# Kernel tuning notes

Measured on AMD Instinct MI355X. Metric: run time of the kernel, lower is better.

Reference implementation:

```python
import jax, jax.numpy as jnp
import numpy as np

PRIME = 2147483647  # 2^31 - 1, MinHash modulus
GAMMA = 0.3
NUM_HEADS = 8


def minhash_sketch(ids, a, b):
    # ids: (B, L, S) int64 atom ids; a,b: (K,) hash coefficients
    # h[b,l,s,k] = (a[k]*id + b[k]) mod PRIME ; signature = min over the set axis S
    h = (ids[..., None] * a + b) % PRIME          # (B, L, S, K)
    return h.min(axis=2)                          # (B, L, K)


def jaccard_from_signatures(sig_q, sig_k):
    # sig_q: (B, Lq, K), sig_k: (B, Lk, K) -> (B, Lq, Lk) fraction of matching slots.
    # Scan over the K hash slots to avoid materializing a (B,Lq,Lk,K) tensor.
    B, Lq, K = sig_q.shape
    Lk = sig_k.shape[1]

    def step(acc, cols):
        qc, kc = cols                              # (B,Lq), (B,Lk)
        return acc + (qc[:, :, None] == kc[:, None, :]).astype(jnp.float32), None

    init = jnp.zeros((B, Lq, Lk), jnp.float32)
    xs = (jnp.moveaxis(sig_q, -1, 0), jnp.moveaxis(sig_k, -1, 0))
    acc, _ = jax.lax.scan(step, init, xs)
    return acc / K


def symdiff_from_jaccard(jacc, size_q, size_k):
    # |A ∩ B| = J/(1+J) * (|A|+|B|)  =>  |A Δ B| = (|A|+|B|) * (1-J)/(1+J)
    tot = size_q[:, :, None] + size_k[:, None, :]   # (B, Lq, Lk)
    return tot * (1.0 - jacc) / (1.0 + jacc)


def setup_inputs() -> dict:
    key = jax.random.key(0)
    ks = jax.random.split(key, 12)
    B, Lq, Lk, E, S, K, V = 4, 1024, 1024, 512, 8, 128, 32000
    w = lambda k: (jax.random.normal(k, (E, E), jnp.float32) * 0.02)
    return {
        "query": jax.random.normal(ks[0], (B, Lq, E), jnp.float32),
        "key": jax.random.normal(ks[1], (B, Lk, E), jnp.float32),
        "value": jax.random.normal(ks[2], (B, Lk, E), jnp.float32),
        "token_sets_q": jax.random.randint(ks[3], (B, Lq, S), 0, V).astype(jnp.int64),
        "token_sets_k": jax.random.randint(ks[4], (B, Lk, S), 0, V).astype(jnp.int64),
        "hash_a": jax.random.randint(ks[5], (K,), 1, PRIME - 1).astype(jnp.int64),
        "hash_b": jax.random.randint(ks[6], (K,), 0, PRIME - 1).astype(jnp.int64),
        "Wq": w(ks[7]), "bq": jnp.zeros((E,), jnp.float32),
        "Wk": w(ks[8]), "bk": jnp.zeros((E,), jnp.float32),
        "Wv": w(ks[9]), "bv": jnp.zeros((E,), jnp.float32),
        "Wo": w(ks[10]), "bo": jnp.zeros((E,), jnp.float32),
    }


def reference(query, key, value, token_sets_q, token_sets_k, hash_a, hash_b,
              Wq, bq, Wk, bk, Wv, bv, Wo, bo):
    B, Lq, E = query.shape
    Lk = key.shape[1]
    H = NUM_HEADS
    d = E // H

    # in-projections (torch Linear: x @ W^T + b); q,k are computed but the
    # attention scores come solely from the token-set kernel (gating disabled)
    q = query @ Wq.T + bq
    k = key @ Wk.T + bk
    v = (value @ Wv.T + bv).reshape(B, Lk, H, d).transpose(0, 2, 1, 3)  # (B,H,Lk,d)

    # MinHash sketches of per-token atom sets -> estimated Jaccard -> Δ-RBF score
    sig_q = minhash_sketch(token_sets_q, hash_a, hash_b)   # (B,Lq,K)
    sig_k = minhash_sketch(token_sets_k, hash_a, hash_b)   # (B,Lk,K)
    jacc = jaccard_from_signatures(sig_q, sig_k)           # (B,Lq,Lk)

    S = token_sets_q.shape[-1]
    size_q = jnp.full((B, Lq), S, jnp.float32)             # uniform CSR offsets -> |set| = S
    size_k = jnp.full((B, Lk), S, jnp.float32)
    delta = symdiff_from_jaccard(jacc, size_q, size_k)
    scores = jnp.exp(-GAMMA * delta)                       # (B,Lq,Lk), shared by all heads

    attn = jax.nn.softmax(scores, axis=-1)                 # no masks, no causal, dropout=0
    ctx = jnp.einsum('bqk,bhkd->bqhd', attn, v).reshape(B, Lq, E)
    return ctx @ Wo.T + bo
```

## Files before the change

### kernel.cpp

```cpp
#include <hip/hip_runtime.h>
#include <hip/hip_bf16.h>
#include <stdint.h>

#define PRIME 2147483647u
#define GAMMA 0.3f
#define K_HASH 128
#define S_SET 8
#define NB 4
#define LQ 1024
#define LK 1024
#define EDIM 512

typedef unsigned short ushort_t;
typedef __attribute__((ext_vector_type(8))) short short8;
typedef __attribute__((ext_vector_type(4))) float f32x4;

static __device__ __forceinline__ unsigned short f2bf(float f) {
    unsigned u = __builtin_bit_cast(unsigned, f);
    u += 0x7FFFu + ((u >> 16) & 1u);
    return (unsigned short)(u >> 16);
}

static __device__ __forceinline__ void glds16(const void* g, void* l) {
    __builtin_amdgcn_global_load_lds(
        (const __attribute__((address_space(1))) unsigned int*)g,
        (__attribute__((address_space(3))) unsigned int*)l, 16, 0, 0);
}

#define SWZ(r) ((((r) >> 2) & 3) ^ ((r) & 3))

#define EPI_ROWBIAS  0
#define EPI_ROWDIV   1
#define EPI_COLBIAS  2

template<int OUTF32, int MODE>
static __device__ void gemm64_dev(
        const ushort_t* __restrict__ A, const ushort_t* __restrict__ B,
        void* __restrict__ C,
        const float* __restrict__ bias, const float* __restrict__ scale,
        int lda, int ldb, int ldc, int Kd, int m0, int n0,
        ushort_t* AsBase, ushort_t* BsBase, int tid) {
    ushort_t (*As)[64 * 32] = (ushort_t (*)[64 * 32])AsBase;
    ushort_t (*Bs)[64 * 32] = (ushort_t (*)[64 * 32])BsBase;
    int w = tid >> 6, lane = tid & 63;
    int wm = (w & 1) * 32, wn = (w >> 1) * 32;
    int mrow = lane & 15, kg = lane >> 4;

    int r = tid >> 2, c = (tid & 3) ^ SWZ(r);
    const ushort_t* pa = A + (size_t)(m0 + r) * lda + c * 8;
    const ushort_t* pb = B + (size_t)(n0 + r) * ldb + c * 8;

    int aoff[2], boff[2];
    #pragma unroll
    for (int s = 0; s < 2; s++) {
        int Ra = wm + s * 16 + mrow;
        aoff[s] = Ra * 32 + (kg ^ SWZ(Ra)) * 8;
        int Rb = wn + s * 16 + mrow;
        boff[s] = Rb * 32 + (kg ^ SWZ(Rb)) * 8;
    }

    f32x4 acc[2][2] = {};
    int nK = Kd >> 5;
    glds16(pa, &As[0][tid * 8]);
    glds16(pb, &Bs[0][tid * 8]);
    for (int i = 0; i < nK; i++) {
        __syncthreads();
        int cur = i & 1, nxt = cur ^ 1;
        if (i + 1 < nK) {
            int k0 = (i + 1) << 5;
            glds16(pa + k0, &As[nxt][tid * 8]);
            glds16(pb + k0, &Bs[nxt][tid * 8]);
        }
        short8 af[2], bh[2];
        #pragma unroll
        for (int s = 0; s < 2; s++) {
            af[s] = *(const short8*)&As[cur][aoff[s]];
            bh[s] = *(const short8*)&Bs[cur][boff[s]];
        }
        #pragma unroll
        for (int ii = 0; ii < 2; ii++)
            #pragma unroll
            for (int jj = 0; jj < 2; jj++)
                acc[ii][jj] = __builtin_amdgcn_mfma_f32_16x16x32_bf16(
                                  af[ii], bh[jj], acc[ii][jj], 0, 0, 0);
    }

    int col = lane & 15, rbase = (lane >> 4) * 4;
    #pragma unroll
    for (int ii = 0; ii < 2; ii++) {
        #pragma unroll
        for (int jj = 0; jj < 2; jj++) {
            #pragma unroll
            for (int rr = 0; rr < 4; rr++) {
                int gm = m0 + wm + ii * 16 + rbase + rr;
                int gn = n0 + wn + jj * 16 + col;
                float v = acc[ii][jj][rr];
                if (MODE == EPI_ROWBIAS)     v += bias[gm];
                else if (MODE == EPI_ROWDIV) v /= scale[gm];
                else                         v += bias[gn];
                size_t cix = (size_t)gm * ldc + gn;
                if (OUTF32) ((float*)C)[cix] = v;
                else        ((ushort_t*)C)[cix] = f2bf(v);
            }
        }
    }
}

#define CVT_N0 (NB * LK * EDIM)
#define CVT_N1 (EDIM * EDIM)
#define CVT_N2 (EDIM * EDIM)
#define CVT_BLOCKS ((CVT_N0 + CVT_N1 + CVT_N2) / (256 * 8))
#define MZ_BLOCKS 1024
#define SIG_BLOCKS (NB * (LQ + LK) / 2)

__global__ __launch_bounds__(256) void prep_kernel(
        const float* __restrict__ v, const float* __restrict__ wv,
        const float* __restrict__ wo,
        ushort_t* __restrict__ vb, ushort_t* __restrict__ wvb,
        ushort_t* __restrict__ wob,
        const int* __restrict__ ts_q, const int* __restrict__ ts_k,
        const int* __restrict__ ha, const int* __restrict__ hb,
        unsigned* __restrict__ sig_q, unsigned* __restrict__ sig_k,
        uint8_t* __restrict__ Mz) {
    int blk = blockIdx.x;
    if (blk < CVT_BLOCKS) {
        size_t i = ((size_t)blk * 256 + threadIdx.x) * 8;
        const float* src; ushort_t* dst; size_t off;
        if (i < CVT_N0)                { src = v;  dst = vb;  off = i; }
        else if (i < CVT_N0 + CVT_N1)  { src = wv; dst = wvb; off = i - CVT_N0; }
        else                           { src = wo; dst = wob; off = i - CVT_N0 - CVT_N1; }
        float4 a = *(const float4*)(src + off);
        float4 b = *(const float4*)(src + off + 4);
        ushort4 o0, o1;
        o0.x = f2bf(a.x); o0.y = f2bf(a.y); o0.z = f2bf(a.z); o0.w = f2bf(a.w);
        o1.x = f2bf(b.x); o1.y = f2bf(b.y); o1.z = f2bf(b.z); o1.w = f2bf(b.w);
        *(ushort4*)(dst + off)     = o0;
        *(ushort4*)(dst + off + 4) = o1;
        return;
    }
    if (blk < CVT_BLOCKS + MZ_BLOCKS) {
        size_t off = ((size_t)(blk - CVT_BLOCKS) * 256 + threadIdx.x) * 16;
        *(int4*)(Mz + off) = (int4){0, 0, 0, 0};
        return;
    }
    int sb = blk - CVT_BLOCKS - MZ_BLOCKS;
    int half = threadIdx.x >> 7, k = threadIdx.x & 127;
    int row = sb * 2 + half;
    const int* ts = (row < NB * LQ) ? ts_q : ts_k;
    unsigned* sig = (row < NB * LQ) ? sig_q : sig_k;
    int idx = row & (NB * LQ - 1);
    unsigned long long a  = (unsigned)ha[k];
    unsigned long long bb = (unsigned)hb[k];
    __shared__ int ids[2][S_SET];
    if (k < S_SET) ids[half][k] = ts[idx * S_SET + k];
    __syncthreads();
    unsigned mn = 0xFFFFFFFFu;
    #pragma unroll
    for (int s = 0; s < S_SET; s++) {
        unsigned long long x = a * (unsigned long long)(unsigned)ids[half][s] + bb;
        x = (x & PRIME) + (x >> 31);
        x = (x & PRIME) + (x >> 31);
        unsigned r = (unsigned)x;
        if (r >= PRIME) r -= PRIME;
        mn = (r < mn) ? r : mn;
    }
    sig[idx * K_HASH + k] = mn;
}

union JSmem {
    struct { unsigned keys[2048]; ushort_t vals[2048]; } j;
    struct { ushort_t As[2][64 * 32]; ushort_t Bs[2][64 * 32]; } g;
};

__global__ __launch_bounds__(256) void joing1_kernel(
        const unsigned* __restrict__ sig_q, const unsigned* __restrict__ sig_k,
        uint8_t* __restrict__ M,
        const ushort_t* __restrict__ Wvb, const ushort_t* __restrict__ Vb,
        ushort_t* __restrict__ Vt, const float* __restrict__ bv) {
    __shared__ JSmem sm;
    int blk = blockIdx.x, tid = threadIdx.x;
    int t = blk & 511;
    if ((blk >> 9) == 0) {
        gemm64_dev<0, EPI_ROWBIAS>(Wvb, Vb, Vt, bv, nullptr,
                                   EDIM, EDIM, NB * LK, EDIM,
                                   (t >> 6) * 64, (t & 63) * 64,
                                   sm.g.As[0], sm.g.Bs[0], tid);
        return;
    }
    int b = t >> 7, k = t & 127;
    for (int i = tid; i < 2048; i += 256) sm.j.keys[i] = 0xFFFFFFFFu;
    __syncthreads();
    const unsigned* skc = sig_k + (size_t)b * LK * K_HASH + k;
    const unsigned* sqc = sig_q + (size_t)b * LQ * K_HASH + k;
    for (int u = 0; u < 4; u++) {
        int j = u * 256 + tid;
        unsigned vv = skc[(size_t)j * K_HASH];
        unsigned h = (vv * 2654435761u) >> 21;
        while (true) {
            unsigned prev = atomicCAS(&sm.j.keys[h], 0xFFFFFFFFu, vv);
            if (prev == 0xFFFFFFFFu) { sm.j.vals[h] = (ushort_t)j; break; }
            h = (h + 1) & 2047;
        }
    }
    __syncthreads();
    uint8_t* Mb = M + ((size_t)b << 20);
    for (int u = 0; u < 4; u++) {
        int q = u * 256 + tid;
        unsigned vv = sqc[(size_t)q * K_HASH];
        unsigned h = (vv * 2654435761u) >> 21;
        unsigned kk;
        while ((kk = sm.j.keys[h]) != 0xFFFFFFFFu) {
            if (kk == vv) {
                unsigned ix = ((unsigned)q << 10) + sm.j.vals[h];
                atomicAdd((unsigned*)(Mb + (ix & ~3u)), 1u << ((ix & 3u) * 8));
            }
            h = (h + 1) & 2047;
        }
    }
}

__global__ __launch_bounds__(256) void lutrs_kernel(
        const uint8_t* __restrict__ M, ushort_t* __restrict__ P,
        float* __restrict__ rs) {
    __shared__ float lut[K_HASH + 1];
    __shared__ float wsum[4];
    int row = blockIdx.x, tid = threadIdx.x;
    if (tid <= K_HASH) {
        float r = (float)(K_HASH - tid) / (float)(K_HASH + tid);
        lut[tid] = expf(expf(-GAMMA * (2.0f * S_SET) * r));
    }
    __syncthreads();
    uchar4 m4 = *(const uchar4*)(M + (size_t)row * LK + tid * 4);
    float p0 = lut[m4.x], p1 = lut[m4.y], p2 = lut[m4.z], p3 = lut[m4.w];
    ushort4 o;
    o.x = f2bf(p0); o.y = f2bf(p1); o.z = f2bf(p2); o.w = f2bf(p3);
    *(ushort4*)(P + (size_t)row * LK + tid * 4) = o;
    float s = (p0 + p1) + (p2 + p3);
    #pragma unroll
    for (int off = 32; off; off >>= 1) s += __shfl_down(s, off);
    if ((tid & 63) == 0) wsum[tid >> 6] = s;
    __syncthreads();
    if (tid == 0) rs[row] = (wsum[0] + wsum[1]) + (wsum[2] + wsum[3]);
}

template<int OUTF32, int MODE>
__global__ __launch_bounds__(256) void btgemm_kernel(
        const ushort_t* __restrict__ A, const ushort_t* __restrict__ B,
        void* __restrict__ C,
        const float* __restrict__ bias, const float* __restrict__ scale,
        int lda, int ldb, int ldc, int Kd,
        long long sA, long long sB, long long sC, long long sS) {
    __shared__ ushort_t As[2][64 * 32], Bs[2][64 * 32];
    int z = blockIdx.z;
    gemm64_dev<OUTF32, MODE>(
        A + (size_t)z * sA, B + (size_t)z * sB,
        (char*)C + (size_t)z * sC * (OUTF32 ? 4 : 2),
        bias, scale + (size_t)z * sS,
        lda, ldb, ldc, Kd, blockIdx.y * 64, blockIdx.x * 64,
        As[0], Bs[0], threadIdx.x);
}

extern "C" void kernel_launch(void* const* d_in, const int* in_sizes, int n_in,
                              void* d_out, int out_size, void* d_ws, size_t ws_size,
                              hipStream_t stream) {
    const float* value = (const float*)d_in[2];
    const int* tsq = (const int*)d_in[3];
    const int* tsk = (const int*)d_in[4];
    const int* ha  = (const int*)d_in[5];
    const int* hb  = (const int*)d_in[6];
    const float* Wv = (const float*)d_in[11];
    const float* bv = (const float*)d_in[12];
    const float* Wo = (const float*)d_in[13];
    const float* bo = (const float*)d_in[14];
    float* out = (float*)d_out;

    char* ws = (char*)d_ws;
    unsigned* sigq = (unsigned*)(ws);
    unsigned* sigk = (unsigned*)(ws + (2ull << 20));
    uint8_t*  M    = (uint8_t*)(ws + (4ull << 20));
    ushort_t* P    = (ushort_t*)(ws + (8ull << 20));
    float*    rs   = (float*)(ws + (16ull << 20));
    ushort_t* Vt   = (ushort_t*)(ws + (16ull << 20) + (64ull << 10));
    ushort_t* ctx  = (ushort_t*)(ws);
    ushort_t* Vb   = (ushort_t*)(ws + (20ull << 20) + (64ull << 10));
    ushort_t* Wvb  = (ushort_t*)(ws + (24ull << 20) + (64ull << 10));
    ushort_t* Wob  = (ushort_t*)(ws + (24ull << 20) + (64ull << 10) + (512ull << 10));

    prep_kernel<<<CVT_BLOCKS + MZ_BLOCKS + SIG_BLOCKS, 256, 0, stream>>>(
        value, Wv, Wo, Vb, Wvb, Wob, tsq, tsk, ha, hb, sigq, sigk, M);

    joing1_kernel<<<1024, 256, 0, stream>>>(sigq, sigk, M, Wvb, Vb, Vt, bv);

    lutrs_kernel<<<NB * LQ, 256, 0, stream>>>(M, P, rs);

    btgemm_kernel<0, EPI_ROWDIV><<<dim3(EDIM / 64, LQ / 64, NB), 256, 0, stream>>>(
        P, Vt, ctx, bv , rs,
        LK, NB * LK, EDIM, LK,
        (long long)LQ * LK, (long long)LK, (long long)LQ * EDIM, (long long)LQ);

    btgemm_kernel<1, EPI_COLBIAS><<<dim3(EDIM / 64, NB * LQ / 64, 1), 256, 0, stream>>>(
        ctx, Wob, out, bo, rs ,
        EDIM, EDIM, EDIM, EDIM, 0LL, 0LL, 0LL, 0LL);
}
```

Baseline: 151.4 us.

## Fold Wo into V projection and replace dense LUT pass with sparse fixups

Reassociates the output projection so that Wo·(Wv·V) is precomputed as W2t, which removes the separate ctx GEMM; the score GEMM then writes the final fp32 output with a divide-by-rowsum plus bias epilogue. P and rowsums are prefilled with the zero-match score. The join records the first hit of each nonzero match cell in a fixlist, and a sparse fixup pass patches P and rowsums, replacing the dense LUT/rowsum kernel. The join also loads four hash slots per block with vector loads. This adds atomics on a global counter and a large fixlist buffer, and it changes the rounding order (bf16 of W2t and Vproj).

```diff
diff --git a/kernel.cpp b/kernel.cpp
--- a/kernel.cpp
+++ b/kernel.cpp
@@ -10,6 +10,7 @@
 #define LQ 1024
 #define LK 1024
 #define EDIM 512
+#define FIX_CAP (NB * LQ * LK)
 
 typedef unsigned short ushort_t;
 typedef __attribute__((ext_vector_type(8))) short short8;
@@ -29,9 +30,15 @@
 
 #define SWZ(r) ((((r) >> 2) & 3) ^ ((r) & 3))
 
+static __device__ __forceinline__ float score_of(int m) {
+    float r = (float)(K_HASH - m) / (float)(K_HASH + m);
+    return expf(expf(-GAMMA * (2.0f * S_SET) * r));
+}
+
 #define EPI_ROWBIAS  0
-#define EPI_ROWDIV   1
 #define EPI_COLBIAS  2
+#define EPI_NONE     3
+#define EPI_DIVBIAS  4
 
 template<int OUTF32, int MODE>
 static __device__ void gemm64_dev(
@@ -95,9 +102,9 @@
                 int gm = m0 + wm + ii * 16 + rbase + rr;
                 int gn = n0 + wn + jj * 16 + col;
                 float v = acc[ii][jj][rr];
-                if (MODE == EPI_ROWBIAS)     v += bias[gm];
-                else if (MODE == EPI_ROWDIV) v /= scale[gm];
-                else                         v += bias[gn];
+                if (MODE == EPI_ROWBIAS)      v += bias[gm];
+                else if (MODE == EPI_COLBIAS) v += bias[gn];
+                else if (MODE == EPI_DIVBIAS) v = v / scale[gm] + bias[gn];
                 size_t cix = (size_t)gm * ldc + gn;
                 if (OUTF32) ((float*)C)[cix] = v;
                 else        ((ushort_t*)C)[cix] = f2bf(v);
@@ -110,8 +117,11 @@
 #define CVT_N1 (EDIM * EDIM)
 #define CVT_N2 (EDIM * EDIM)
 #define CVT_BLOCKS ((CVT_N0 + CVT_N1 + CVT_N2) / (256 * 8))
+#define PF_BLOCKS 2048
 #define MZ_BLOCKS 1024
+#define RS_BLOCKS 16
 #define SIG_BLOCKS (NB * (LQ + LK) / 2)
+#define PREP_GRID (CVT_BLOCKS + PF_BLOCKS + MZ_BLOCKS + RS_BLOCKS + SIG_BLOCKS)
 
 __global__ __launch_bounds__(256) void prep_kernel(
         const float* __restrict__ v, const float* __restrict__ wv,
@@ -121,7 +131,8 @@
         const int* __restrict__ ts_q, const int* __restrict__ ts_k,
         const int* __restrict__ ha, const int* __restrict__ hb,
         unsigned* __restrict__ sig_q, unsigned* __restrict__ sig_k,
-        uint8_t* __restrict__ Mz) {
+        uint8_t* __restrict__ M, ushort_t* __restrict__ P,
+        float* __restrict__ rs, unsigned* __restrict__ nfix) {
     int blk = blockIdx.x;
     if (blk < CVT_BLOCKS) {
         size_t i = ((size_t)blk * 256 + threadIdx.x) * 8;
@@ -138,12 +149,25 @@
         *(ushort4*)(dst + off + 4) = o1;
         return;
     }
-    if (blk < CVT_BLOCKS + MZ_BLOCKS) {
+    if (blk < CVT_BLOCKS + PF_BLOCKS) {
+        unsigned short pb = f2bf(score_of(0));
+        unsigned wpat = (unsigned)pb | ((unsigned)pb << 16);
         size_t off = ((size_t)(blk - CVT_BLOCKS) * 256 + threadIdx.x) * 16;
-        *(int4*)(Mz + off) = (int4){0, 0, 0, 0};
-        return;
-    }
-    int sb = blk - CVT_BLOCKS - MZ_BLOCKS;
+        *(int4*)((char*)P + off) = (int4){(int)wpat, (int)wpat, (int)wpat, (int)wpat};
+        return;
+    }
+    if (blk < CVT_BLOCKS + PF_BLOCKS + MZ_BLOCKS) {
+        size_t off = ((size_t)(blk - CVT_BLOCKS - PF_BLOCKS) * 256 + threadIdx.x) * 16;
+        *(int4*)(M + off) = (int4){0, 0, 0, 0};
+        return;
+    }
+    if (blk < CVT_BLOCKS + PF_BLOCKS + MZ_BLOCKS + RS_BLOCKS) {
+        int i = (blk - CVT_BLOCKS - PF_BLOCKS - MZ_BLOCKS) * 256 + threadIdx.x;
+        rs[i] = (float)LK * score_of(0);
+        if (i == 0) *nfix = 0u;
+        return;
+    }
+    int sb = blk - (CVT_BLOCKS + PF_BLOCKS + MZ_BLOCKS + RS_BLOCKS);
     int half = threadIdx.x >> 7, k = threadIdx.x & 127;
     int row = sb * 2 + half;
     const int* ts = (row < NB * LQ) ? ts_q : ts_k;
@@ -172,75 +196,105 @@
     struct { ushort_t As[2][64 * 32]; ushort_t Bs[2][64 * 32]; } g;
 };
 
+static __device__ __forceinline__ unsigned vc4(int4 v, int c) {
+    return (unsigned)(c == 0 ? v.x : c == 1 ? v.y : c == 2 ? v.z : v.w);
+}
+
 __global__ __launch_bounds__(256) void joing1_kernel(
         const unsigned* __restrict__ sig_q, const unsigned* __restrict__ sig_k,
-        uint8_t* __restrict__ M,
+        uint8_t* __restrict__ M, unsigned* __restrict__ fixlist,
+        unsigned* __restrict__ nfix,
         const ushort_t* __restrict__ Wvb, const ushort_t* __restrict__ Vb,
-        ushort_t* __restrict__ Vt, const float* __restrict__ bv) {
+        ushort_t* __restrict__ Vproj, const float* __restrict__ bv) {
     __shared__ JSmem sm;
     int blk = blockIdx.x, tid = threadIdx.x;
-    int t = blk & 511;
-    if ((blk >> 9) == 0) {
-        gemm64_dev<0, EPI_ROWBIAS>(Wvb, Vb, Vt, bv, nullptr,
-                                   EDIM, EDIM, NB * LK, EDIM,
-                                   (t >> 6) * 64, (t & 63) * 64,
+    int r5 = blk % 5;
+    if (r5 < 4) {
+        int t = (blk / 5) * 4 + r5;
+        gemm64_dev<0, EPI_COLBIAS>(Vb, Wvb, Vproj, bv, nullptr,
+                                   EDIM, EDIM, EDIM, EDIM,
+                                   (t >> 3) * 64, (t & 7) * 64,
                                    sm.g.As[0], sm.g.Bs[0], tid);
         return;
     }
-    int b = t >> 7, k = t & 127;
-    for (int i = tid; i < 2048; i += 256) sm.j.keys[i] = 0xFFFFFFFFu;
-    __syncthreads();
-    const unsigned* skc = sig_k + (size_t)b * LK * K_HASH + k;
-    const unsigned* sqc = sig_q + (size_t)b * LQ * K_HASH + k;
+    int jt = blk / 5;
+    int b = jt >> 5, kg = jt & 31;
+    const int4* skb = (const int4*)(sig_k + (size_t)b * LK * K_HASH + kg * 4);
+    const int4* sqb = (const int4*)(sig_q + (size_t)b * LQ * K_HASH + kg * 4);
+    int4 kv[4], qv[4];
+    #pragma unroll
     for (int u = 0; u < 4; u++) {
-        int j = u * 256 + tid;
-        unsigned vv = skc[(size_t)j * K_HASH];
-        unsigned h = (vv * 2654435761u) >> 21;
-        while (true) {
-            unsigned prev = atomicCAS(&sm.j.keys[h], 0xFFFFFFFFu, vv);
-            if (prev == 0xFFFFFFFFu) { sm.j.vals[h] = (ushort_t)j; break; }
-            h = (h + 1) & 2047;
-        }
-    }
-    __syncthreads();
+        int row = u * 256 + tid;
+        kv[u] = skb[(size_t)row * (K_HASH / 4)];
+        qv[u] = sqb[(size_t)row * (K_HASH / 4)];
+    }
     uint8_t* Mb = M + ((size_t)b << 20);
-    for (int u = 0; u < 4; u++) {
-        int q = u * 256 + tid;
-        unsigned vv = sqc[(size_t)q * K_HASH];
-        unsigned h = (vv * 2654435761u) >> 21;
-        unsigned kk;
-        while ((kk = sm.j.keys[h]) != 0xFFFFFFFFu) {
-            if (kk == vv) {
-                unsigned ix = ((unsigned)q << 10) + sm.j.vals[h];
-                atomicAdd((unsigned*)(Mb + (ix & ~3u)), 1u << ((ix & 3u) * 8));
+    #pragma unroll
+    for (int c = 0; c < 4; c++) {
+        __syncthreads();
+        for (int i = tid; i < 2048; i += 256) sm.j.keys[i] = 0xFFFFFFFFu;
+        __syncthreads();
+        #pragma unroll
+        for (int u = 0; u < 4; u++) {
+            int j = u * 256 + tid;
+            unsigned vv = vc4(kv[u], c);
+            unsigned h = (vv * 2654435761u) >> 21;
+            while (true) {
+                unsigned prev = atomicCAS(&sm.j.keys[h], 0xFFFFFFFFu, vv);
+                if (prev == 0xFFFFFFFFu) { sm.j.vals[h] = (ushort_t)j; break; }
+                h = (h + 1) & 2047;
             }
-            h = (h + 1) & 2047;
-        }
-    }
-}
-
-__global__ __launch_bounds__(256) void lutrs_kernel(
-        const uint8_t* __restrict__ M, ushort_t* __restrict__ P,
-        float* __restrict__ rs) {
-    __shared__ float lut[K_HASH + 1];
-    __shared__ float wsum[4];
-    int row = blockIdx.x, tid = threadIdx.x;
-    if (tid <= K_HASH) {
-        float r = (float)(K_HASH - tid) / (float)(K_HASH + tid);
-        lut[tid] = expf(expf(-GAMMA * (2.0f * S_SET) * r));
-    }
-    __syncthreads();
-    uchar4 m4 = *(const uchar4*)(M + (size_t)row * LK + tid * 4);
-    float p0 = lut[m4.x], p1 = lut[m4.y], p2 = lut[m4.z], p3 = lut[m4.w];
-    ushort4 o;
-    o.x = f2bf(p0); o.y = f2bf(p1); o.z = f2bf(p2); o.w = f2bf(p3);
-    *(ushort4*)(P + (size_t)row * LK + tid * 4) = o;
-    float s = (p0 + p1) + (p2 + p3);
-    #pragma unroll
-    for (int off = 32; off; off >>= 1) s += __shfl_down(s, off);
-    if ((tid & 63) == 0) wsum[tid >> 6] = s;
-    __syncthreads();
-    if (tid == 0) rs[row] = (wsum[0] + wsum[1]) + (wsum[2] + wsum[3]);
+        }
+        __syncthreads();
+        #pragma unroll
+        for (int u = 0; u < 4; u++) {
+            int q = u * 256 + tid;
+            unsigned vv = vc4(qv[u], c);
+            unsigned h = (vv * 2654435761u) >> 21, kk;
+            while ((kk = sm.j.keys[h]) != 0xFFFFFFFFu) {
+                if (kk == vv) {
+                    unsigned ix = ((unsigned)q << 10) + sm.j.vals[h];
+                    unsigned sh = (ix & 3u) * 8;
+                    unsigned old = atomicAdd((unsigned*)(Mb + (ix & ~3u)), 1u << sh);
+                    if (((old >> sh) & 0xFFu) == 0u) {
+                        unsigned slot = atomicAdd(nfix, 1u);
+                        if (slot < (unsigned)FIX_CAP)
+                            fixlist[slot] = ((unsigned)b << 20) | ix;
+                    }
+                }
+                h = (h + 1) & 2047;
+            }
+        }
+    }
+}
+
+__global__ __launch_bounds__(256) void g1bfix_kernel(
+        const ushort_t* __restrict__ Wob, const ushort_t* __restrict__ Vproj,
+        ushort_t* __restrict__ W2t,
+        const uint8_t* __restrict__ M, const unsigned* __restrict__ fixlist,
+        const unsigned* __restrict__ nfix,
+        ushort_t* __restrict__ P, float* __restrict__ rs) {
+    __shared__ ushort_t As[2][64 * 32], Bs[2][64 * 32];
+    int blk = blockIdx.x, tid = threadIdx.x;
+    if (blk < 512) {
+        gemm64_dev<0, EPI_NONE>(Wob, Vproj, W2t, nullptr, nullptr,
+                                EDIM, EDIM, NB * LK, EDIM,
+                                (blk >> 6) * 64, (blk & 63) * 64,
+                                As[0], Bs[0], tid);
+        return;
+    }
+    unsigned n = *nfix;
+    if (n > (unsigned)FIX_CAP) n = FIX_CAP;
+    float p0 = score_of(0);
+    for (unsigned i = (unsigned)(blk - 512) * 256 + tid; i < n; i += 64 * 256) {
+        unsigned e = fixlist[i];
+        int b = e >> 20;
+        unsigned ix = e & 0xFFFFFu;
+        int m = M[((size_t)b << 20) + ix];
+        float p = score_of(m);
+        P[((size_t)b << 20) + ix] = f2bf(p);
+        atomicAdd(&rs[(b << 10) + (ix >> 10)], p - p0);
+    }
 }
 
 template<int OUTF32, int MODE>
@@ -275,30 +329,31 @@
     float* out = (float*)d_out;
 
     char* ws = (char*)d_ws;
-    unsigned* sigq = (unsigned*)(ws);
-    unsigned* sigk = (unsigned*)(ws + (2ull << 20));
-    uint8_t*  M    = (uint8_t*)(ws + (4ull << 20));
-    ushort_t* P    = (ushort_t*)(ws + (8ull << 20));
-    float*    rs   = (float*)(ws + (16ull << 20));
-    ushort_t* Vt   = (ushort_t*)(ws + (16ull << 20) + (64ull << 10));
-    ushort_t* ctx  = (ushort_t*)(ws);
-    ushort_t* Vb   = (ushort_t*)(ws + (20ull << 20) + (64ull << 10));
-    ushort_t* Wvb  = (ushort_t*)(ws + (24ull << 20) + (64ull << 10));
-    ushort_t* Wob  = (ushort_t*)(ws + (24ull << 20) + (64ull << 10) + (512ull << 10));
-
-    prep_kernel<<<CVT_BLOCKS + MZ_BLOCKS + SIG_BLOCKS, 256, 0, stream>>>(
-        value, Wv, Wo, Vb, Wvb, Wob, tsq, tsk, ha, hb, sigq, sigk, M);
-
-    joing1_kernel<<<1024, 256, 0, stream>>>(sigq, sigk, M, Wvb, Vb, Vt, bv);
-
-    lutrs_kernel<<<NB * LQ, 256, 0, stream>>>(M, P, rs);
-
-    btgemm_kernel<0, EPI_ROWDIV><<<dim3(EDIM / 64, LQ / 64, NB), 256, 0, stream>>>(
-        P, Vt, ctx, bv , rs,
+    unsigned* sigq  = (unsigned*)(ws);
+    unsigned* sigk  = (unsigned*)(ws + (2ull << 20));
+    uint8_t*  M     = (uint8_t*)(ws + (4ull << 20));
+    ushort_t* P     = (ushort_t*)(ws + (8ull << 20));
+    float*    rs    = (float*)(ws + (16ull << 20));
+    unsigned* nfix  = (unsigned*)(ws + (16ull << 20) + (32ull << 10));
+    unsigned* fixl  = (unsigned*)(ws + (17ull << 20));
+    ushort_t* Vproj = (ushort_t*)(ws + (33ull << 20));
+    ushort_t* W2t   = (ushort_t*)(ws + (37ull << 20));
+    ushort_t* Vb    = (ushort_t*)(ws + (41ull << 20));
+    ushort_t* Wvb   = (ushort_t*)(ws + (45ull << 20));
+    ushort_t* Wob   = (ushort_t*)(ws + (45ull << 20) + (512ull << 10));
+
+    prep_kernel<<<PREP_GRID, 256, 0, stream>>>(
+        value, Wv, Wo, Vb, Wvb, Wob, tsq, tsk, ha, hb, sigq, sigk,
+        M, P, rs, nfix);
+
+    joing1_kernel<<<640, 256, 0, stream>>>(
+        sigq, sigk, M, fixl, nfix, Wvb, Vb, Vproj, bv);
+
+    g1bfix_kernel<<<576, 256, 0, stream>>>(
+        Wob, Vproj, W2t, M, fixl, nfix, P, rs);
+
+    btgemm_kernel<1, EPI_DIVBIAS><<<dim3(EDIM / 64, LQ / 64, NB), 256, 0, stream>>>(
+        P, W2t, out, bo, rs,
         LK, NB * LK, EDIM, LK,
         (long long)LQ * LK, (long long)LK, (long long)LQ * EDIM, (long long)LQ);
-
-    btgemm_kernel<1, EPI_COLBIAS><<<dim3(EDIM / 64, NB * LQ / 64, 1), 256, 0, stream>>>(
-        ctx, Wob, out, bo, rs ,
-        EDIM, EDIM, EDIM, EDIM, 0LL, 0LL, 0LL, 0LL);
-}
+}
```

New measurement: 213.2 us. 1.41x slower.
